# Optimization experiments

Measured on AMD Instinct MI355X. Metric: run time of the kernel, lower is better.

## Reference

```python
import jax, jax.numpy as jnp
import numpy as np

NUM_LAYERS = 8
REL_SIZE = 16      # heads per layer
KEY_SIZE = 64
HIDDEN = REL_SIZE * KEY_SIZE  # 1024


def _mass_sincos(node_mass):
    # Sinusoidal embedding of scalar mass -> [B, N, 1, KEY_SIZE]
    half = KEY_SIZE // 2
    inv_freq = jnp.exp(-jnp.log(jnp.float32(10000.0)) * jnp.arange(half, dtype=jnp.float32) / half)
    ang = node_mass[..., None, None] * inv_freq  # [B, N, 1, half]
    return jnp.sin(ang), jnp.cos(ang)


def setup_inputs() -> dict:
    key = jax.random.key(0)
    k1, k2, k3, k4 = jax.random.split(key, 4)
    B, N = 4, 2048
    out_dim = HIDDEN * NUM_LAYERS * 2  # 16384
    node = jax.random.normal(k1, (B, N, HIDDEN), dtype=jnp.float32)
    node_mass = jax.random.uniform(k2, (B, N), dtype=jnp.float32) * 100.0
    W = jax.random.normal(k3, (HIDDEN, out_dim), dtype=jnp.float32) * (1.0 / np.sqrt(HIDDEN))
    b = jax.random.normal(k4, (out_dim,), dtype=jnp.float32) * 0.02
    return {"node": node, "node_mass": node_mass, "W": W, "b": b}


def reference(node, node_mass, W, b):
    B, N, _ = node.shape
    H = REL_SIZE * NUM_LAYERS  # heads per cache (k or v)
    # Fused KV projection: [B, N, 2*H, KEY_SIZE]
    kv = (jnp.einsum('bnh,ho->bno', node, W) + b).reshape(B, N, 2 * H, KEY_SIZE)
    k_cache, v_cache = kv[:, :, :H, :], kv[:, :, H:, :]
    # Rotary-style rotation of k_cache by mass sin/cos (broadcast over heads)
    dis_sin, dis_cos = _mass_sincos(node_mass)      # each [B, N, 1, KEY_SIZE//2]
    half = KEY_SIZE // 2
    x0, x1 = k_cache[..., :half], k_cache[..., half:]
    k_cache = jnp.concatenate([x0 * dis_cos - x1 * dis_sin,
                               x0 * dis_sin + x1 * dis_cos], axis=-1)
    # transpose(1, 2): [B, H, N, KEY_SIZE]; per-layer chunks are contiguous slices
    k_out = jnp.swapaxes(k_cache, 1, 2)
    v_out = jnp.swapaxes(v_cache, 1, 2)
    # Stack K and V caches; layer chunks = slices of size REL_SIZE along head dim
    return jnp.stack([k_out, v_out], axis=0)  # [2, B, H, N, KEY_SIZE]
```

## Files before the change

### kernel.cpp

```cpp
#include <hip/hip_runtime.h>
#include <stdint.h>

#define M_TOT 8192
#define N_TOT 16384
#define K_TOT 1024

typedef __bf16 bf16x8 __attribute__((ext_vector_type(8)));
typedef float f32x4 __attribute__((ext_vector_type(4)));

__device__ __forceinline__ unsigned short f2bf(float f) {
  unsigned int u = __float_as_uint(f);
  u = u + 0x7FFFu + ((u >> 16) & 1u);
  return (unsigned short)(u >> 16);
}

__device__ __forceinline__ void gload_lds16(const void* g, void* l) {
  __builtin_amdgcn_global_load_lds(
      (const __attribute__((address_space(1))) unsigned int*)g,
      (__attribute__((address_space(3))) unsigned int*)l,
      16, 0, 0);
}

__global__ __launch_bounds__(256) void k_convert_node(
    const float* __restrict__ src, unsigned short* __restrict__ dst) {
  size_t base = ((size_t)blockIdx.x * 256 + threadIdx.x) * 8;
#pragma unroll
  for (int it = 0; it < 4; it++) {
    size_t i = base + (size_t)it * (1024 * 256 * 8);
    float4 v0 = *(const float4*)(src + i);
    float4 v1 = *(const float4*)(src + i + 4);
    union { unsigned short u[8]; uint4 q; } r;
    r.u[0] = f2bf(v0.x); r.u[1] = f2bf(v0.y); r.u[2] = f2bf(v0.z); r.u[3] = f2bf(v0.w);
    r.u[4] = f2bf(v1.x); r.u[5] = f2bf(v1.y); r.u[6] = f2bf(v1.z); r.u[7] = f2bf(v1.w);
    *(uint4*)(dst + i) = r.q;
  }
}

__global__ __launch_bounds__(256) void k_transpose_w(
    const float* __restrict__ W, unsigned short* __restrict__ Wt) {
  __shared__ float tile[64][65];
  int o0 = blockIdx.x * 64;
  int k0 = blockIdx.y * 64;
  int t = threadIdx.x;
  int kr0 = t >> 4, c4 = t & 15;
#pragma unroll
  for (int i = 0; i < 4; i++) {
    int kr = kr0 + i * 16;
    float4 v = *(const float4*)&W[(size_t)(k0 + kr) * N_TOT + o0 + c4 * 4];
    tile[kr][c4 * 4 + 0] = v.x;
    tile[kr][c4 * 4 + 1] = v.y;
    tile[kr][c4 * 4 + 2] = v.z;
    tile[kr][c4 * 4 + 3] = v.w;
  }
  __syncthreads();
  int or0 = t >> 3, c8 = t & 7;
#pragma unroll
  for (int i = 0; i < 2; i++) {
    int orr = or0 + i * 32;
    union { unsigned short u[8]; uint4 q; } r;
#pragma unroll
    for (int j = 0; j < 8; j++) r.u[j] = f2bf(tile[c8 * 8 + j][orr]);
    *(uint4*)&Wt[(size_t)(o0 + orr) * K_TOT + k0 + c8 * 8] = r.q;
  }
}

__global__ __launch_bounds__(256) void k_sincos(
    const float* __restrict__ mass, float* __restrict__ sin_t, float* __restrict__ cos_t) {
  int t = blockIdx.x * 256 + threadIdx.x;
  int row = t >> 5;
  int d = t & 31;
  float m = mass[row];
  float invf = expf(-0.28782313662425575f * (float)d);
  float ang = m * invf;
  float s, c;
  sincosf(ang, &s, &c);
  sin_t[t] = s;
  cos_t[t] = c;
}

__global__ __launch_bounds__(256, 2) void k_gemm256b(
    const unsigned short* __restrict__ A,
    const unsigned short* __restrict__ Bt,
    const float* __restrict__ bias,
    const float* __restrict__ sin_t,
    const float* __restrict__ cos_t,
    float* __restrict__ out)
{
  extern __shared__ char smem[];

  int tid  = threadIdx.x;
  int lane = tid & 63;
  int wid  = tid >> 6;
  int wm   = wid >> 1;
  int wn   = wid & 1;

  int orig = blockIdx.x;
  int x   = orig & 7;
  int c   = orig >> 3;
  int st  = c >> 5;
  int w   = c & 31;
  int bm0 = (x * 4 + (w >> 3)) * 256;
  int bn0 = (st * 8 + (w & 7)) * 128;

  int sv   = (tid & 7) ^ ((tid >> 3) & 7);
  int arow = ((tid >> 3) << 1) + (sv >> 2);
  int kst  = sv & 3;
  const unsigned short* srcA = A  + (size_t)(bm0 + arow) * K_TOT + kst * 8;
  const unsigned short* srcB = Bt + (size_t)(bn0 + arow) * K_TOT + kst * 8;
  const size_t rs64 = (size_t)64 * K_TOT;

  int wofs = wid * 1024;

#define STAGE_A(s_, bo_) do { char* dA = smem + (bo_) + wofs; \
    const unsigned short* sa = srcA + (size_t)(s_) * 32; \
    gload_lds16(sa,            dA); \
    gload_lds16(sa + rs64,     dA + 4096); \
    gload_lds16(sa + 2 * rs64, dA + 8192); \
    gload_lds16(sa + 3 * rs64, dA + 12288); } while (0)
#define STAGE_B(s_, bo_) do { char* dB = smem + (bo_) + 16384 + wofs; \
    const unsigned short* sb = srcB + (size_t)(s_) * 32; \
    gload_lds16(sb,        dB); \
    gload_lds16(sb + rs64, dB + 4096); } while (0)

  STAGE_A(0, 0); STAGE_B(0, 0);
  STAGE_A(1, 24576); STAGE_B(1, 24576);

  f32x4 acc[8][4] = {};

  int r = lane & 15;
  int q = lane >> 4;
  int sl   = (((r & 1) << 2) + q) ^ ((r >> 1) & 7);
  int aoff = wm * 8192 + (r >> 1) * 128 + sl * 16;
  int boff = wn * 4096 + (r >> 1) * 128 + sl * 16;

  int cur = 0;
  int stg = 49152;

  for (int s = 0; s < 32; ++s) {
    if (s < 31) { asm volatile("s_waitcnt vmcnt(6)" ::: "memory"); }
    else        { asm volatile("s_waitcnt vmcnt(0)" ::: "memory"); }
    __builtin_amdgcn_s_barrier();
    __builtin_amdgcn_sched_barrier(0);

    const char* As_ = smem + cur;
    const char* Bs_ = As_ + 16384;

    bf16x8 bfrag[4], afrag[4];
#pragma unroll
    for (int ni = 0; ni < 4; ni++) bfrag[ni] = *(const bf16x8*)(Bs_ + boff + ni * 1024);
#pragma unroll
    for (int mi = 0; mi < 4; mi++) afrag[mi] = *(const bf16x8*)(As_ + aoff + mi * 1024);
    if (s < 30) STAGE_A(s + 2, stg);
    __builtin_amdgcn_s_setprio(1);
#pragma unroll
    for (int mi = 0; mi < 4; mi++)
#pragma unroll
      for (int ni = 0; ni < 4; ni++)
        acc[mi][ni] = __builtin_amdgcn_mfma_f32_16x16x32_bf16(afrag[mi], bfrag[ni], acc[mi][ni], 0, 0, 0);
    __builtin_amdgcn_s_setprio(0);

    bf16x8 afrag2[4];
#pragma unroll
    for (int mi = 0; mi < 4; mi++) afrag2[mi] = *(const bf16x8*)(As_ + aoff + (mi + 4) * 1024);
    if (s < 30) STAGE_B(s + 2, stg);
    __builtin_amdgcn_s_setprio(1);
#pragma unroll
    for (int mi = 0; mi < 4; mi++)
#pragma unroll
      for (int ni = 0; ni < 4; ni++)
        acc[mi + 4][ni] = __builtin_amdgcn_mfma_f32_16x16x32_bf16(afrag2[mi], bfrag[ni], acc[mi + 4][ni], 0, 0, 0);
    __builtin_amdgcn_s_setprio(0);

    stg = cur;
    cur = (cur == 49152) ? 0 : cur + 24576;
  }
#undef STAGE_A
#undef STAGE_B

  int col16 = r;
  float bv[4];
#pragma unroll
  for (int ni = 0; ni < 4; ni++) bv[ni] = bias[bn0 + wn * 64 + ni * 16 + col16];

  int cgrp = (bn0 >> 6) + wn;
  int is_k = (cgrp < 128);
  int h = cgrp & 127;
  size_t sec = is_k ? 0 : 4;

#pragma unroll
  for (int mi = 0; mi < 8; mi++) {
#pragma unroll
    for (int reg = 0; reg < 4; reg++) {
      int row = bm0 + wm * 128 + mi * 16 + q * 4 + reg;
      int bb = row >> 11;
      int n  = row & 2047;
      float* op = out + (((sec + bb) * 128 + h) * 2048 + (size_t)n) * 64;
      if (is_k) {
#pragma unroll
        for (int ni = 0; ni < 2; ni++) {
          int d = ni * 16 + col16;
          float x0 = acc[mi][ni][reg]     + bv[ni];
          float x1 = acc[mi][ni + 2][reg] + bv[ni + 2];
          float sv = sin_t[row * 32 + d];
          float cv = cos_t[row * 32 + d];
          op[d]      = x0 * cv - x1 * sv;
          op[d + 32] = x0 * sv + x1 * cv;
        }
      } else {
#pragma unroll
        for (int ni = 0; ni < 4; ni++) {
          int d = ni * 16 + col16;
          op[d] = acc[mi][ni][reg] + bv[ni];
        }
      }
    }
  }
}

extern "C" void kernel_launch(void* const* d_in, const int* in_sizes, int n_in,
                              void* d_out, int out_size, void* d_ws, size_t ws_size,
                              hipStream_t stream) {
  const float* node = (const float*)d_in[0];
  const float* mass = (const float*)d_in[1];
  const float* W    = (const float*)d_in[2];
  const float* bias = (const float*)d_in[3];
  float* out = (float*)d_out;

  const size_t NODE_B  = (size_t)M_TOT * K_TOT * 2;
  const size_t WT_B    = (size_t)N_TOT * K_TOT * 2;
  const size_t SIN_B   = (size_t)M_TOT * 32 * 4;
  if (ws_size < NODE_B + WT_B + 2 * SIN_B) return;

  char* ws = (char*)d_ws;
  unsigned short* nodeB = (unsigned short*)ws;
  unsigned short* WtB   = (unsigned short*)(ws + NODE_B);
  float* sin_t = (float*)(ws + NODE_B + WT_B);
  float* cos_t = (float*)(ws + NODE_B + WT_B + SIN_B);

  (void)hipFuncSetAttribute((const void*)k_gemm256b,
                            hipFuncAttributeMaxDynamicSharedMemorySize, 73728);

  k_convert_node<<<1024, 256, 0, stream>>>(node, nodeB);
  k_transpose_w<<<dim3(N_TOT / 64, K_TOT / 64), 256, 0, stream>>>(W, WtB);
  k_sincos<<<(M_TOT * 32) / 256, 256, 0, stream>>>(mass, sin_t, cos_t);
  k_gemm256b<<<dim3((M_TOT / 256) * (N_TOT / 128)), dim3(256), 73728, stream>>>(
      nodeB, WtB, bias, sin_t, cos_t, out);
}
```

Before: 357.1 us.

## Double-buffer LDS fragments in registers across GEMM main-loop iterations

Restructures the bf16 MFMA main loop so each iteration prefetches the next stage's A(0-3) and B fragments from LDS into a second register set, while computing on the current set. The loop is unrolled by two to ping-pong the register buffers. Global-to-LDS staging for both A and B of stage s+2 is now issued together at the top of each iteration. Each iteration now waits for all outstanding global loads (vmcnt(0)), which shrinks the prefetch distance. The extra fragment registers also raise VGPR pressure under a two-waves-per-SIMD launch bound.

```diff
diff --git a/kernel.cpp b/kernel.cpp
--- a/kernel.cpp
+++ b/kernel.cpp
@@ -122,9 +122,6 @@
     gload_lds16(sb,        dB); \
     gload_lds16(sb + rs64, dB + 4096); } while (0)
 
-  STAGE_A(0, 0); STAGE_B(0, 0);
-  STAGE_A(1, 24576); STAGE_B(1, 24576);
-
   f32x4 acc[8][4] = {};
 
   int r = lane & 15;
@@ -133,47 +130,61 @@
   int aoff = wm * 8192 + (r >> 1) * 128 + sl * 16;
   int boff = wn * 4096 + (r >> 1) * 128 + sl * 16;
 
-  int cur = 0;
-  int stg = 49152;
-
-  for (int s = 0; s < 32; ++s) {
-    if (s < 31) { asm volatile("s_waitcnt vmcnt(6)" ::: "memory"); }
-    else        { asm volatile("s_waitcnt vmcnt(0)" ::: "memory"); }
-    __builtin_amdgcn_s_barrier();
-    __builtin_amdgcn_sched_barrier(0);
-
-    const char* As_ = smem + cur;
-    const char* Bs_ = As_ + 16384;
-
-    bf16x8 bfrag[4], afrag[4];
-#pragma unroll
-    for (int ni = 0; ni < 4; ni++) bfrag[ni] = *(const bf16x8*)(Bs_ + boff + ni * 1024);
-#pragma unroll
-    for (int mi = 0; mi < 4; mi++) afrag[mi] = *(const bf16x8*)(As_ + aoff + mi * 1024);
-    if (s < 30) STAGE_A(s + 2, stg);
-    __builtin_amdgcn_s_setprio(1);
-#pragma unroll
-    for (int mi = 0; mi < 4; mi++)
-#pragma unroll
-      for (int ni = 0; ni < 4; ni++)
-        acc[mi][ni] = __builtin_amdgcn_mfma_f32_16x16x32_bf16(afrag[mi], bfrag[ni], acc[mi][ni], 0, 0, 0);
-    __builtin_amdgcn_s_setprio(0);
-
-    bf16x8 afrag2[4];
-#pragma unroll
-    for (int mi = 0; mi < 4; mi++) afrag2[mi] = *(const bf16x8*)(As_ + aoff + (mi + 4) * 1024);
-    if (s < 30) STAGE_B(s + 2, stg);
-    __builtin_amdgcn_s_setprio(1);
-#pragma unroll
-    for (int mi = 0; mi < 4; mi++)
-#pragma unroll
-      for (int ni = 0; ni < 4; ni++)
-        acc[mi + 4][ni] = __builtin_amdgcn_mfma_f32_16x16x32_bf16(afrag2[mi], bfrag[ni], acc[mi + 4][ni], 0, 0, 0);
-    __builtin_amdgcn_s_setprio(0);
-
-    stg = cur;
-    cur = (cur == 49152) ? 0 : cur + 24576;
-  }
+  STAGE_A(0, 0); STAGE_B(0, 0);
+  STAGE_A(1, 24576); STAGE_B(1, 24576);
+  asm volatile("s_waitcnt vmcnt(6)" ::: "memory");
+  __builtin_amdgcn_s_barrier();
+  __builtin_amdgcn_sched_barrier(0);
+
+  bf16x8 bX[4], aX[4], bY[4], aY[4];
+#pragma unroll
+  for (int ni = 0; ni < 4; ni++) bX[ni] = *(const bf16x8*)(smem + 16384 + boff + ni * 1024);
+#pragma unroll
+  for (int mi = 0; mi < 4; mi++) aX[mi] = *(const bf16x8*)(smem + aoff + mi * 1024);
+
+  int cur = 0, nxt = 24576, stg = 49152;
+
+#define GEMM_ITER(s_, BC, A03C, BN, A03N) do {                                  \
+    asm volatile("s_waitcnt vmcnt(0)" ::: "memory");                            \
+    __builtin_amdgcn_s_barrier();                                               \
+    __builtin_amdgcn_sched_barrier(0);                                          \
+    if ((s_) < 30) { STAGE_A((s_) + 2, stg); STAGE_B((s_) + 2, stg); }          \
+    const char* As_ = smem + cur;                                               \
+    const char* Asn = smem + nxt;                                               \
+    bf16x8 a47[4];                                                              \
+    _Pragma("unroll")                                                           \
+    for (int mi = 0; mi < 4; mi++)                                              \
+      a47[mi] = *(const bf16x8*)(As_ + aoff + (mi + 4) * 1024);                 \
+    if ((s_) < 31) {                                                            \
+      _Pragma("unroll")                                                         \
+      for (int ni = 0; ni < 4; ni++)                                            \
+        BN[ni] = *(const bf16x8*)(Asn + 16384 + boff + ni * 1024);              \
+      _Pragma("unroll")                                                         \
+      for (int mi = 0; mi < 4; mi++)                                            \
+        A03N[mi] = *(const bf16x8*)(Asn + aoff + mi * 1024);                    \
+    }                                                                           \
+    __builtin_amdgcn_s_setprio(1);                                              \
+    _Pragma("unroll")                                                           \
+    for (int mi = 0; mi < 4; mi++)                                              \
+      _Pragma("unroll")                                                         \
+      for (int ni = 0; ni < 4; ni++)                                            \
+        acc[mi][ni] = __builtin_amdgcn_mfma_f32_16x16x32_bf16(                  \
+            A03C[mi], BC[ni], acc[mi][ni], 0, 0, 0);                            \
+    _Pragma("unroll")                                                           \
+    for (int mi = 0; mi < 4; mi++)                                              \
+      _Pragma("unroll")                                                         \
+      for (int ni = 0; ni < 4; ni++)                                            \
+        acc[mi + 4][ni] = __builtin_amdgcn_mfma_f32_16x16x32_bf16(              \
+            a47[mi], BC[ni], acc[mi + 4][ni], 0, 0, 0);                         \
+    __builtin_amdgcn_s_setprio(0);                                              \
+    int t_ = cur; cur = nxt; nxt = stg; stg = t_;                               \
+  } while (0)
+
+  for (int s2 = 0; s2 < 32; s2 += 2) {
+    GEMM_ITER(s2,     bX, aX, bY, aY);
+    GEMM_ITER(s2 + 1, bY, aY, bX, aX);
+  }
+#undef GEMM_ITER
 #undef STAGE_A
 #undef STAGE_B
 
@@ -201,10 +212,10 @@
           int d = ni * 16 + col16;
           float x0 = acc[mi][ni][reg]     + bv[ni];
           float x1 = acc[mi][ni + 2][reg] + bv[ni + 2];
-          float sv = sin_t[row * 32 + d];
-          float cv = cos_t[row * 32 + d];
-          op[d]      = x0 * cv - x1 * sv;
-          op[d + 32] = x0 * sv + x1 * cv;
+          float sv2 = sin_t[row * 32 + d];
+          float cv2 = cos_t[row * 32 + d];
+          op[d]      = x0 * cv2 - x1 * sv2;
+          op[d + 32] = x0 * sv2 + x1 * cv2;
         }
       } else {
 #pragma unroll
```

Result: slower. 368.9 us (+3.3%).
